# Kernel tuning notes

Measured on AMD Instinct MI355X. Metric: run time of the kernel, lower is better.

The kernel has to match this reference:

```python
import jax, jax.numpy as jnp
import numpy as np

B, N, DIM = 1, 2048, 2048
H, KVH = 32, 4                 # query heads, kv heads
D = DIM // H                   # head_dim = 64
REP = H // KVH                 # queries per kv = 8
KV_DIM = D * KVH               # 256


def _rope_tables(n, d, base=10000.0):
    inv = 1.0 / (base ** (np.arange(0, d, 2, dtype=np.float32) / d))
    t = np.arange(n, dtype=np.float32)
    freqs = np.outer(t, inv)                      # [n, d/2]
    emb = np.concatenate([freqs, freqs], axis=-1)  # [n, d]
    return jnp.asarray(np.cos(emb)), jnp.asarray(np.sin(emb))


def setup_inputs() -> dict:
    key = jax.random.key(0)
    ks = jax.random.split(key, 5)
    s = 0.02
    cos, sin = _rope_tables(N, D)
    return {
        "x": jax.random.normal(ks[0], (B, N, DIM), jnp.float32),
        "Wq": jax.random.normal(ks[1], (DIM, DIM), jnp.float32) * s,
        "Wk": jax.random.normal(ks[2], (KV_DIM, DIM), jnp.float32) * s,
        "Wv": jax.random.normal(ks[3], (KV_DIM, DIM), jnp.float32) * s,
        "Wo": jax.random.normal(ks[4], (DIM, DIM), jnp.float32) * s,
        "cos": cos,
        "sin": sin,
    }


def _rotate_half(t):
    d2 = t.shape[-1] // 2
    return jnp.concatenate([-t[..., d2:], t[..., :d2]], axis=-1)


def reference(x, Wq, Wk, Wv, Wo, cos, sin):
    b, n, _ = x.shape
    # projections (nn.Linear: x @ W.T)
    q = (x @ Wq.T).reshape(b, n, H, D).transpose(0, 2, 1, 3)     # b h n d
    k = (x @ Wk.T).reshape(b, n, KVH, D).transpose(0, 2, 1, 3)   # b g n d
    v = (x @ Wv.T).reshape(b, n, KVH, D).transpose(0, 2, 1, 3)
    # RoPE
    c = cos[None, None, :, :]
    s = sin[None, None, :, :]
    q = q * c + _rotate_half(q) * s
    k = k * c + _rotate_half(k) * s
    # expand KV heads (repeat_interleave over head dim)
    k = jnp.repeat(k, REP, axis=1)   # b h n d
    v = jnp.repeat(v, REP, axis=1)
    # causal attention with materialized scores (faithful to source)
    scale = 1.0 / jnp.sqrt(jnp.asarray(D, x.dtype))
    scores = jnp.einsum('bhld,bhsd->bhls', q, k) * scale
    causal = jnp.tril(jnp.ones((n, n), bool))
    scores = jnp.where(causal[None, None], scores, jnp.asarray(-jnp.inf, x.dtype))
    attn = jax.nn.softmax(scores, axis=-1)
    y = jnp.einsum('bhls,bhsd->bhld', attn, v)       # b h n d
    y = y.transpose(0, 2, 1, 3).reshape(b, n, DIM)   # b n (h d)
    return y @ Wo.T
```

## Files before the change

kernel.cpp:

```cpp
#include <hip/hip_runtime.h>

typedef unsigned short u16;
typedef __attribute__((ext_vector_type(8))) short short8;
typedef __attribute__((ext_vector_type(4))) float floatx4;

#define N_TOK 2048
#define DIM   2048
#define NH    32
#define NKVH  4
#define HD    64
#define KVD   256

__device__ __forceinline__ float bf2f(u16 u) {
  union { unsigned i; float f; } c; c.i = ((unsigned)u) << 16; return c.f;
}
__device__ __forceinline__ u16 f2bf(float f) {
  union { float f; unsigned i; } c; c.f = f;
  unsigned x = c.i;
  return (u16)((x + 0x7fffu + ((x >> 16) & 1u)) >> 16);
}

__device__ __forceinline__ void gload16(const u16* g, u16* l) {
#if defined(__has_builtin) && __has_builtin(__builtin_amdgcn_global_load_lds)
  __builtin_amdgcn_global_load_lds(
      (const __attribute__((address_space(1))) void*)g,
      (__attribute__((address_space(3))) void*)l, 16, 0, 0);
#else
  *(short8*)l = *(const short8*)g;
#endif
}

#define C_X  1048576
#define C_WQ 2097152
#define C_WK 2228224
#define C_WV 2359296
#define C_WO 3407872
__global__ __launch_bounds__(256) void cvt_all(const float* __restrict__ x,
                                               const float* __restrict__ wq,
                                               const float* __restrict__ wk,
                                               const float* __restrict__ wv,
                                               const float* __restrict__ wo,
                                               u16* __restrict__ dst) {
  int i = blockIdx.x * 256 + threadIdx.x;
  const float* src; int off;
  if      (i < C_X)  { src = x;  off = 0; }
  else if (i < C_WQ) { src = wq; off = C_X; }
  else if (i < C_WK) { src = wk; off = C_WQ; }
  else if (i < C_WV) { src = wv; off = C_WK; }
  else               { src = wo; off = C_WV; }
  float4 v = ((const float4*)src)[i - off];
  ushort4 o;
  o.x = f2bf(v.x); o.y = f2bf(v.y); o.z = f2bf(v.z); o.w = f2bf(v.w);
  ((ushort4*)dst)[i] = o;
}


__global__ __launch_bounds__(256) void gemm_qkv(const u16* __restrict__ A,
                                                const u16* __restrict__ Wq,
                                                const u16* __restrict__ Wk,
                                                const u16* __restrict__ Wv,
                                                const float* __restrict__ cs,
                                                const float* __restrict__ sn,
                                                u16* __restrict__ Qp,
                                                u16* __restrict__ Kp,
                                                u16* __restrict__ Vp) {
  __shared__ __align__(16) u16 As[64 * 32];
  __shared__ __align__(16) u16 Bs[128 * 32];
  const int tid  = threadIdx.x;
  const int lane = tid & 63;
  const int w    = tid >> 6;
  const int r    = lane & 15, q = lane >> 4;
  const int tm = blockIdx.x & 31;
  const int tn = blockIdx.x >> 5;
  const int wm = w & 1, wn = w >> 1;
  const int K = DIM;

  const u16* W; int wrow0;
  if (tn < 16)      { W = Wq; wrow0 = tn * 128; }
  else if (tn < 18) { W = Wk; wrow0 = (tn - 16) * 128; }
  else              { W = Wv; wrow0 = (tn - 18) * 128; }

  const int srow = tid >> 2;
  const int scol = (tid & 3) * 8;
  const u16* ga = A + (size_t)(tm * 64 + srow) * K + scol;
  const u16* gb = W + (size_t)(wrow0 + srow) * K + scol;
  u16* lA = &As[tid * 8];
  u16* lB = &Bs[tid * 8];

  floatx4 acc[2][4];
#pragma unroll
  for (int a = 0; a < 2; ++a)
#pragma unroll
    for (int b = 0; b < 4; ++b) acc[a][b] = (floatx4){0.f, 0.f, 0.f, 0.f};

  for (int k0 = 0; k0 < K; k0 += 32) {
    __syncthreads();
    gload16(ga + k0, lA);
    gload16(gb + k0, lB);
    gload16(gb + k0 + (size_t)64 * K, lB + 2048);
    __syncthreads();

    short8 af[2], bf[4];
#pragma unroll
    for (int mi = 0; mi < 2; ++mi)
      af[mi] = *(const short8*)&As[(wm * 32 + mi * 16 + r) * 32 + q * 8];
#pragma unroll
    for (int nj = 0; nj < 4; ++nj)
      bf[nj] = *(const short8*)&Bs[(wn * 64 + nj * 16 + r) * 32 + q * 8];
#pragma unroll
    for (int mi = 0; mi < 2; ++mi)
#pragma unroll
      for (int nj = 0; nj < 4; ++nj)
        acc[mi][nj] = __builtin_amdgcn_mfma_f32_16x16x32_bf16(af[mi], bf[nj], acc[mi][nj], 0, 0, 0);
  }

  if (tn < 18) {
    const int head = (tn < 16) ? (tn * 2 + wn) : ((tn - 16) * 2 + wn);
#pragma unroll
    for (int mi = 0; mi < 2; ++mi)
#pragma unroll
      for (int g = 0; g < 4; ++g) {
        int row = tm * 64 + wm * 32 + mi * 16 + 4 * q + g;
        const float* crow  = cs + (size_t)row * 64;
        const float* srow2 = sn + (size_t)row * 64;
#pragma unroll
        for (int nj = 0; nj < 2; ++nj) {
          int d = nj * 16 + r;
          float x0 = acc[mi][nj][g];
          float x1 = acc[mi][nj + 2][g];
          float o0 = x0 * crow[d]      - x1 * srow2[d];
          float o1 = x1 * crow[d + 32] + x0 * srow2[d + 32];
          int qq = d >> 3, j = d & 7;
          int lslot = (qq * 16 + (row & 15)) * 8 + j;
          if (tn < 16) {
            int sq = row >> 5, ii = (row >> 4) & 1;
            size_t base = ((size_t)(head * 64 + sq) * 4 + ii * 2) * 512 + lslot;
            Qp[base]       = f2bf(o0);
            Qp[base + 512] = f2bf(o1);
          } else {
            int kt = row >> 6, t = (row >> 4) & 3;
            size_t base = ((size_t)(head * 32 + kt) * 8 + t * 2) * 512 + lslot;
            Kp[base]       = f2bf(o0);
            Kp[base + 512] = f2bf(o1);
          }
        }
      }
  } else {
#pragma unroll
    for (int mi = 0; mi < 2; ++mi)
#pragma unroll
      for (int nj = 0; nj < 4; ++nj) {
        int col  = (tn - 18) * 128 + wn * 64 + nj * 16 + r;
        int kvh  = col >> 6;
        int t    = (col & 63) >> 4;
        int rr   = col & 15;
        int row0 = tm * 64 + wm * 32 + mi * 16 + 4 * q;
        int kt   = row0 >> 6;
        int wk   = row0 & 63;
        int s    = wk >> 5;
        int qq   = (wk & 31) >> 3;
        int j0   = wk & 7;
        uint2 pk;
        pk.x = (unsigned)f2bf(acc[mi][nj][0]) | ((unsigned)f2bf(acc[mi][nj][1]) << 16);
        pk.y = (unsigned)f2bf(acc[mi][nj][2]) | ((unsigned)f2bf(acc[mi][nj][3]) << 16);
        size_t idx = ((size_t)(kvh * 32 + kt) * 8 + s * 4 + t) * 512 + (qq * 16 + rr) * 8 + j0;
        *(uint2*)(Vp + idx) = pk;
      }
  }
}

__global__ __launch_bounds__(256) void gemm_out(const u16* __restrict__ A,
                                                const u16* __restrict__ W,
                                                float* __restrict__ C) {
  __shared__ __align__(16) u16 As[64 * 32];
  __shared__ __align__(16) u16 Bs[128 * 32];
  const int tid  = threadIdx.x;
  const int lane = tid & 63;
  const int w    = tid >> 6;
  const int r    = lane & 15, q = lane >> 4;
  const int tn = blockIdx.x & 15;
  const int tm = blockIdx.x >> 4;
  const int wm = w & 1, wn = w >> 1;
  const int K = DIM;

  const int srow = tid >> 2;
  const int scol = (tid & 3) * 8;
  const u16* ga = A + (size_t)(tm * 64 + srow) * K + scol;
  const u16* gb = W + (size_t)(tn * 128 + srow) * K + scol;
  u16* lA = &As[tid * 8];
  u16* lB = &Bs[tid * 8];

  floatx4 acc[2][4];
#pragma unroll
  for (int a = 0; a < 2; ++a)
#pragma unroll
    for (int b = 0; b < 4; ++b) acc[a][b] = (floatx4){0.f, 0.f, 0.f, 0.f};

  for (int k0 = 0; k0 < K; k0 += 32) {
    __syncthreads();
    gload16(ga + k0, lA);
    gload16(gb + k0, lB);
    gload16(gb + k0 + (size_t)64 * K, lB + 2048);
    __syncthreads();

    short8 af[2], bf[4];
#pragma unroll
    for (int mi = 0; mi < 2; ++mi)
      af[mi] = *(const short8*)&As[(wm * 32 + mi * 16 + r) * 32 + q * 8];
#pragma unroll
    for (int nj = 0; nj < 4; ++nj)
      bf[nj] = *(const short8*)&Bs[(wn * 64 + nj * 16 + r) * 32 + q * 8];
#pragma unroll
    for (int mi = 0; mi < 2; ++mi)
#pragma unroll
      for (int nj = 0; nj < 4; ++nj)
        acc[mi][nj] = __builtin_amdgcn_mfma_f32_16x16x32_bf16(af[mi], bf[nj], acc[mi][nj], 0, 0, 0);
  }

#pragma unroll
  for (int mi = 0; mi < 2; ++mi)
#pragma unroll
    for (int g = 0; g < 4; ++g) {
      int row = tm * 64 + wm * 32 + mi * 16 + 4 * q + g;
#pragma unroll
      for (int nj = 0; nj < 4; ++nj)
        C[(size_t)row * DIM + tn * 128 + wn * 64 + nj * 16 + r] = acc[mi][nj][g];
    }
}

__global__ __launch_bounds__(128, 2) void attn_mfma(const u16* __restrict__ Qp,
                                                    const u16* __restrict__ Kp,
                                                    const u16* __restrict__ Vp,
                                                    u16* __restrict__ Yb) {
  __shared__ __align__(16) u16 Pl[2][32][72];
  __shared__ float Ocmb[32][66];
  __shared__ float Lcmb[2][64];
  const int tid  = threadIdx.x;
  const int lane = tid & 63;
  const int w    = tid >> 6;
  const int r    = lane & 15;
  const int q    = lane >> 4;
  const int bx   = blockIdx.x;
  const int qt   = 15 - (bx >> 2);
  const int sub  = 3 - (bx & 3);
  const int h    = blockIdx.y;
  const int kvh  = h >> 3;
  const int baseq = qt * 128 + sub * 32;
  const int sq   = baseq >> 5;
  const int ktmax = (baseq + 31) >> 6;

  short8 qf[2][2];
#pragma unroll
  for (int i = 0; i < 2; ++i)
#pragma unroll
    for (int c = 0; c < 2; ++c)
      qf[i][c] = *(const short8*)(Qp + ((size_t)(h * 64 + sq) * 4 + i * 2 + c) * 512 + lane * 8);

  floatx4 O[2][4];
  float lsum[2];
#pragma unroll
  for (int i = 0; i < 2; ++i) {
    lsum[i] = 0.f;
#pragma unroll
    for (int t = 0; t < 4; ++t) O[i][t] = (floatx4){0.f, 0.f, 0.f, 0.f};
  }

  const u16* Kbase = Kp + (size_t)(kvh * 32) * 8 * 512;
  const u16* Vbase = Vp + (size_t)(kvh * 32) * 8 * 512;

  auto loadK = [&](int kt, short8 (&kf)[4][2]) {
    const u16* kb = Kbase + (size_t)kt * 8 * 512 + lane * 8;
#pragma unroll
    for (int t = 0; t < 4; ++t) {
      kf[t][0] = *(const short8*)(kb + (t * 2 + 0) * 512);
      kf[t][1] = *(const short8*)(kb + (t * 2 + 1) * 512);
    }
  };

  auto body = [&](int kt, short8 (&kc)[4][2], short8 (&kn)[4][2]) {
    short8 vb[2][4];
    {
      const u16* vbp = Vbase + (size_t)kt * 8 * 512 + lane * 8;
#pragma unroll
      for (int s = 0; s < 2; ++s)
#pragma unroll
        for (int t = 0; t < 4; ++t)
          vb[s][t] = *(const short8*)(vbp + (s * 4 + t) * 512);
    }

    loadK(kt + 2 <= ktmax ? kt + 2 : ktmax, kn);

    floatx4 ST[2][4];
#pragma unroll
    for (int i = 0; i < 2; ++i)
#pragma unroll
      for (int t = 0; t < 4; ++t) ST[i][t] = (floatx4){0.f, 0.f, 0.f, 0.f};
#pragma unroll
    for (int t = 0; t < 4; ++t)
#pragma unroll
      for (int i = 0; i < 2; ++i) {
        ST[i][t] = __builtin_amdgcn_mfma_f32_16x16x32_bf16(kc[t][0], qf[i][0], ST[i][t], 0, 0, 0);
        ST[i][t] = __builtin_amdgcn_mfma_f32_16x16x32_bf16(kc[t][1], qf[i][1], ST[i][t], 0, 0, 0);
      }

    if (kt == ktmax) {
#pragma unroll
      for (int i = 0; i < 2; ++i) {
        int qrow = baseq + 16 * i + r;
#pragma unroll
        for (int t = 0; t < 4; ++t) {
          int key = kt * 64 + 16 * t + 4 * q;
#pragma unroll
          for (int g = 0; g < 4; ++g)
            if (key + g > qrow) ST[i][t][g] = -1e30f;
        }
      }
    }

#pragma unroll
    for (int i = 0; i < 2; ++i)
#pragma unroll
      for (int t = 0; t < 4; ++t) {
        float p0 = __expf(0.125f * ST[i][t][0]);
        float p1 = __expf(0.125f * ST[i][t][1]);
        float p2 = __expf(0.125f * ST[i][t][2]);
        float p3 = __expf(0.125f * ST[i][t][3]);
        lsum[i] += (p0 + p1) + (p2 + p3);
        uint2 pk;
        pk.x = (unsigned)f2bf(p0) | ((unsigned)f2bf(p1) << 16);
        pk.y = (unsigned)f2bf(p2) | ((unsigned)f2bf(p3) << 16);
        *(uint2*)&Pl[w][16 * i + r][16 * t + 4 * q] = pk;
      }

#pragma unroll
    for (int s = 0; s < 2; ++s)
#pragma unroll
      for (int i = 0; i < 2; ++i) {
        short8 pa = *(const short8*)&Pl[w][16 * i + r][32 * s + 8 * q];
#pragma unroll
        for (int t = 0; t < 4; ++t)
          O[i][t] = __builtin_amdgcn_mfma_f32_16x16x32_bf16(pa, vb[s][t], O[i][t], 0, 0, 0);
      }
  };

  short8 kA[4][2], kB[4][2];
  const int kt0 = w;
  if (kt0 <= ktmax) {
    loadK(kt0, kA);
    for (int kt = kt0; kt <= ktmax; kt += 4) {
      body(kt, kA, kB);
      if (kt + 2 <= ktmax) body(kt + 2, kB, kA);
    }
  }

  if (w == 1) {
#pragma unroll
    for (int i = 0; i < 2; ++i) {
#pragma unroll
      for (int t = 0; t < 4; ++t)
#pragma unroll
        for (int g = 0; g < 4; ++g)
          Ocmb[(i * 4 + t) * 4 + g][lane] = O[i][t][g];
      Lcmb[i][lane] = lsum[i];
    }
  }
  __syncthreads();
  if (w == 1) return;
#pragma unroll
  for (int i = 0; i < 2; ++i) {
#pragma unroll
    for (int t = 0; t < 4; ++t)
#pragma unroll
      for (int g = 0; g < 4; ++g)
        O[i][t][g] += Ocmb[(i * 4 + t) * 4 + g][lane];
    lsum[i] += Lcmb[i][lane];
  }

#pragma unroll
  for (int i = 0; i < 2; ++i) {
    lsum[i] += __shfl_xor(lsum[i], 16);
    lsum[i] += __shfl_xor(lsum[i], 32);
  }

#pragma unroll
  for (int i = 0; i < 2; ++i) {
    float inv[4];
#pragma unroll
    for (int g = 0; g < 4; ++g)
      inv[g] = 1.f / __shfl(lsum[i], 4 * q + g);
#pragma unroll
    for (int g = 0; g < 4; ++g) {
      u16* yp = Yb + (size_t)(baseq + 16 * i + 4 * q + g) * DIM + h * 64 + r;
      yp[0]  = f2bf(O[i][0][g] * inv[g]);
      yp[16] = f2bf(O[i][1][g] * inv[g]);
      yp[32] = f2bf(O[i][2][g] * inv[g]);
      yp[48] = f2bf(O[i][3][g] * inv[g]);
    }
  }
}

extern "C" void kernel_launch(void* const* d_in, const int* in_sizes, int n_in,
                              void* d_out, int out_size, void* d_ws, size_t ws_size,
                              hipStream_t stream) {
  const float* x  = (const float*)d_in[0];
  const float* Wq = (const float*)d_in[1];
  const float* Wk = (const float*)d_in[2];
  const float* Wv = (const float*)d_in[3];
  const float* Wo = (const float*)d_in[4];
  const float* cs = (const float*)d_in[5];
  const float* sn = (const float*)d_in[6];

  u16* ws  = (u16*)d_ws;
  u16* xb  = ws;
  u16* Wqb = xb  + (size_t)N_TOK * DIM;
  u16* Wkb = Wqb + (size_t)DIM * DIM;
  u16* Wvb = Wkb + (size_t)KVD * DIM;
  u16* Wob = Wvb + (size_t)KVD * DIM;
  u16* Qp  = Wob + (size_t)DIM * DIM;
  u16* Kp  = Qp  + (size_t)N_TOK * DIM;
  u16* Vp  = Kp  + (size_t)N_TOK * KVD;
  u16* Yb  = Vp  + (size_t)N_TOK * KVD;

  cvt_all<<<dim3(13312), 256, 0, stream>>>(x, Wq, Wk, Wv, Wo, ws);

  gemm_qkv<<<dim3(640), 256, 0, stream>>>(xb, Wqb, Wkb, Wvb, cs, sn, Qp, Kp, Vp);

  attn_mfma<<<dim3(64, 32), 128, 0, stream>>>(Qp, Kp, Vp, Yb);

  gemm_out<<<dim3(512), 256, 0, stream>>>(Yb, Wob, (float*)d_out);
}
```

Measured before the change: 224.0 us.

## Pair complementary causal query blocks per workgroup to balance attention work

Each attention workgroup now processes two 32-row query blocks, one from the end and one from the start of the sequence (j and 63-j), so every block does roughly equal causal work. The grid halves to 32x32 blocks, and each wave splits K tiles across both blocks, with the second block's start parity chosen to balance the two waves. The combine step uses two shared buffers so wave 0 finalizes block A and wave 1 finalizes block B. This trades the tail imbalance of the descending-order schedule for fewer blocks, more registers (two Q/O sets) and more shared memory, which may reduce occupancy.

Result: faster. 207.4 us (-7.4%).

```diff
diff --git a/kernel.cpp b/kernel.cpp
--- a/kernel.cpp
+++ b/kernel.cpp
@@ -233,36 +233,42 @@
                                                     const u16* __restrict__ Vp,
                                                     u16* __restrict__ Yb) {
   __shared__ __align__(16) u16 Pl[2][32][72];
-  __shared__ float Ocmb[32][66];
-  __shared__ float Lcmb[2][64];
+  __shared__ float OcA[32][66];
+  __shared__ float OcB[32][66];
+  __shared__ float LcA[2][64], LcB[2][64];
   const int tid  = threadIdx.x;
   const int lane = tid & 63;
   const int w    = tid >> 6;
   const int r    = lane & 15;
   const int q    = lane >> 4;
-  const int bx   = blockIdx.x;
-  const int qt   = 15 - (bx >> 2);
-  const int sub  = 3 - (bx & 3);
+  const int p    = blockIdx.x;
   const int h    = blockIdx.y;
   const int kvh  = h >> 3;
-  const int baseq = qt * 128 + sub * 32;
-  const int sq   = baseq >> 5;
-  const int ktmax = (baseq + 31) >> 6;
-
-  short8 qf[2][2];
+  const int jA   = 63 - p;
+  const int jB   = p;
+  const int baseqA = jA * 32, baseqB = jB * 32;
+  const int tA = (jA >> 1) + 1, tB = (jB >> 1) + 1;
+  const int ktmaxA = tA - 1, ktmaxB = tB - 1;
+
+  short8 qfA[2][2], qfB[2][2];
 #pragma unroll
   for (int i = 0; i < 2; ++i)
 #pragma unroll
-    for (int c = 0; c < 2; ++c)
-      qf[i][c] = *(const short8*)(Qp + ((size_t)(h * 64 + sq) * 4 + i * 2 + c) * 512 + lane * 8);
-
-  floatx4 O[2][4];
-  float lsum[2];
+    for (int c = 0; c < 2; ++c) {
+      qfA[i][c] = *(const short8*)(Qp + ((size_t)(h * 64 + jA) * 4 + i * 2 + c) * 512 + lane * 8);
+      qfB[i][c] = *(const short8*)(Qp + ((size_t)(h * 64 + jB) * 4 + i * 2 + c) * 512 + lane * 8);
+    }
+
+  floatx4 OA[2][4], OB[2][4];
+  float lsumA[2], lsumB[2];
 #pragma unroll
   for (int i = 0; i < 2; ++i) {
-    lsum[i] = 0.f;
-#pragma unroll
-    for (int t = 0; t < 4; ++t) O[i][t] = (floatx4){0.f, 0.f, 0.f, 0.f};
+    lsumA[i] = 0.f; lsumB[i] = 0.f;
+#pragma unroll
+    for (int t = 0; t < 4; ++t) {
+      OA[i][t] = (floatx4){0.f, 0.f, 0.f, 0.f};
+      OB[i][t] = (floatx4){0.f, 0.f, 0.f, 0.f};
+    }
   }
 
   const u16* Kbase = Kp + (size_t)(kvh * 32) * 8 * 512;
@@ -277,7 +283,9 @@
     }
   };
 
-  auto body = [&](int kt, short8 (&kc)[4][2], short8 (&kn)[4][2]) {
+  auto body = [&](int kt, int ktmax, int baseq,
+                  short8 (&qf)[2][2], floatx4 (&O)[2][4], float (&lsum)[2],
+                  short8 (&kc)[4][2], short8 (&kn)[4][2]) {
     short8 vb[2][4];
     {
       const u16* vbp = Vbase + (size_t)kt * 8 * 512 + lane * 8;
@@ -343,15 +351,20 @@
       }
   };
 
-  short8 kA[4][2], kB[4][2];
-  const int kt0 = w;
-  if (kt0 <= ktmax) {
-    loadK(kt0, kA);
-    for (int kt = kt0; kt <= ktmax; kt += 4) {
-      body(kt, kA, kB);
-      if (kt + 2 <= ktmax) body(kt + 2, kB, kA);
-    }
-  }
+  auto runloop = [&](int start, int ktmax, int baseq,
+                     short8 (&qf)[2][2], floatx4 (&O)[2][4], float (&lsum)[2]) {
+    if (start > ktmax) return;
+    short8 kA[4][2], kB[4][2];
+    loadK(start, kA);
+    for (int kt = start; kt <= ktmax; kt += 4) {
+      body(kt, ktmax, baseq, qf, O, lsum, kA, kB);
+      if (kt + 2 <= ktmax) body(kt + 2, ktmax, baseq, qf, O, lsum, kB, kA);
+    }
+  };
+
+  runloop(w, ktmaxA, baseqA, qfA, OA, lsumA);
+  const int sB = (w + tA) & 1;
+  runloop(sB, ktmaxB, baseqB, qfB, OB, lsumB);
 
   if (w == 1) {
 #pragma unroll
@@ -360,42 +373,67 @@
       for (int t = 0; t < 4; ++t)
 #pragma unroll
         for (int g = 0; g < 4; ++g)
-          Ocmb[(i * 4 + t) * 4 + g][lane] = O[i][t][g];
-      Lcmb[i][lane] = lsum[i];
+          OcA[(i * 4 + t) * 4 + g][lane] = OA[i][t][g];
+      LcA[i][lane] = lsumA[i];
+    }
+  } else {
+#pragma unroll
+    for (int i = 0; i < 2; ++i) {
+#pragma unroll
+      for (int t = 0; t < 4; ++t)
+#pragma unroll
+        for (int g = 0; g < 4; ++g)
+          OcB[(i * 4 + t) * 4 + g][lane] = OB[i][t][g];
+      LcB[i][lane] = lsumB[i];
     }
   }
   __syncthreads();
-  if (w == 1) return;
-#pragma unroll
-  for (int i = 0; i < 2; ++i) {
-#pragma unroll
-    for (int t = 0; t < 4; ++t)
+
+  auto finalize = [&](int baseq, floatx4 (&O)[2][4], float (&lsum)[2]) {
+#pragma unroll
+    for (int i = 0; i < 2; ++i) {
+      lsum[i] += __shfl_xor(lsum[i], 16);
+      lsum[i] += __shfl_xor(lsum[i], 32);
+    }
+#pragma unroll
+    for (int i = 0; i < 2; ++i) {
+      float inv[4];
 #pragma unroll
       for (int g = 0; g < 4; ++g)
-        O[i][t][g] += Ocmb[(i * 4 + t) * 4 + g][lane];
-    lsum[i] += Lcmb[i][lane];
-  }
-
-#pragma unroll
-  for (int i = 0; i < 2; ++i) {
-    lsum[i] += __shfl_xor(lsum[i], 16);
-    lsum[i] += __shfl_xor(lsum[i], 32);
-  }
-
-#pragma unroll
-  for (int i = 0; i < 2; ++i) {
-    float inv[4];
-#pragma unroll
-    for (int g = 0; g < 4; ++g)
-      inv[g] = 1.f / __shfl(lsum[i], 4 * q + g);
-#pragma unroll
-    for (int g = 0; g < 4; ++g) {
-      u16* yp = Yb + (size_t)(baseq + 16 * i + 4 * q + g) * DIM + h * 64 + r;
-      yp[0]  = f2bf(O[i][0][g] * inv[g]);
-      yp[16] = f2bf(O[i][1][g] * inv[g]);
-      yp[32] = f2bf(O[i][2][g] * inv[g]);
-      yp[48] = f2bf(O[i][3][g] * inv[g]);
-    }
+        inv[g] = 1.f / __shfl(lsum[i], 4 * q + g);
+#pragma unroll
+      for (int g = 0; g < 4; ++g) {
+        u16* yp = Yb + (size_t)(baseq + 16 * i + 4 * q + g) * DIM + h * 64 + r;
+        yp[0]  = f2bf(O[i][0][g] * inv[g]);
+        yp[16] = f2bf(O[i][1][g] * inv[g]);
+        yp[32] = f2bf(O[i][2][g] * inv[g]);
+        yp[48] = f2bf(O[i][3][g] * inv[g]);
+      }
+    }
+  };
+
+  if (w == 0) {
+#pragma unroll
+    for (int i = 0; i < 2; ++i) {
+#pragma unroll
+      for (int t = 0; t < 4; ++t)
+#pragma unroll
+        for (int g = 0; g < 4; ++g)
+          OA[i][t][g] += OcA[(i * 4 + t) * 4 + g][lane];
+      lsumA[i] += LcA[i][lane];
+    }
+    finalize(baseqA, OA, lsumA);
+  } else {
+#pragma unroll
+    for (int i = 0; i < 2; ++i) {
+#pragma unroll
+      for (int t = 0; t < 4; ++t)
+#pragma unroll
+        for (int g = 0; g < 4; ++g)
+          OB[i][t][g] += OcB[(i * 4 + t) * 4 + g][lane];
+      lsumB[i] += LcB[i][lane];
+    }
+    finalize(baseqB, OB, lsumB);
   }
 }
 
@@ -425,7 +463,7 @@
 
   gemm_qkv<<<dim3(640), 256, 0, stream>>>(xb, Wqb, Wkb, Wvb, cs, sn, Qp, Kp, Vp);
 
-  attn_mfma<<<dim3(64, 32), 128, 0, stream>>>(Qp, Kp, Vp, Yb);
+  attn_mfma<<<dim3(32, 32), 128, 0, stream>>>(Qp, Kp, Vp, Yb);
 
   gemm_out<<<dim3(512), 256, 0, stream>>>(Yb, Wob, (float*)d_out);
 }
```
